# Performance work log

Measured on AMD Instinct MI355X. Metric: run time of the kernel, lower is better.

## Reference

```python
import jax, jax.numpy as jnp
import numpy as np

B, L, D, H = 4, 4096, 2048, 16
HD = D // H  # head_dim = 128
EPS = 1e-9

def phi(x):
    # ELU(x) + 1 : non-negative feature map
    return jax.nn.elu(x) + 1.0

def setup_inputs() -> dict:
    key = jax.random.key(0)
    k1, k2, k3 = jax.random.split(key, 3)
    x = jax.random.normal(k1, (B, L, D), dtype=jnp.float32)
    W_qkv = jax.random.normal(k2, (3 * D, D), dtype=jnp.float32) * (D ** -0.5)
    W_out = jax.random.normal(k3, (D, D), dtype=jnp.float32) * (D ** -0.5)
    return {"x": x, "W_qkv": W_qkv, "W_out": W_out}

def reference(x, W_qkv, W_out):
    b, l, d = x.shape
    qkv = x @ W_qkv.T                      # (B, L, 3D)
    q, k, v = jnp.split(qkv, 3, axis=-1)   # each (B, L, D)
    # (B, L, H, HD) -> (B, H, L, HD)
    q = q.reshape(b, l, H, HD).transpose(0, 2, 1, 3)
    k = k.reshape(b, l, H, HD).transpose(0, 2, 1, 3)
    v = v.reshape(b, l, H, HD).transpose(0, 2, 1, 3)
    q = phi(q)
    k = phi(k)
    kv_cumsum = jnp.cumsum(k * v, axis=2)  # prefix sum over sequence dim
    k_cumsum = jnp.cumsum(k, axis=2)
    out = q * kv_cumsum / (q * k_cumsum + EPS)
    out = out.transpose(0, 2, 1, 3).reshape(b, l, d)
    return (out @ W_out.T) * (HD ** -0.5)
```

## Files before the change

### kernel.cpp

```cpp
#include <hip/hip_runtime.h>
#include <hip/hip_bf16.h>
#include <stdint.h>

#define B_ 4
#define L_ 4096
#define D_ 2048
#define TD_ (3 * D_)
#define CHUNKS 128
#define CLEN (L_ / CHUNKS)
#define M_ (B_ * L_)
#define K_ 2048
#define NT (K_ / 64)

typedef __bf16 bf16x8 __attribute__((ext_vector_type(8)));
typedef float f32x4 __attribute__((ext_vector_type(4)));
typedef ushort u16x8 __attribute__((ext_vector_type(8)));

__device__ __forceinline__ ushort f2bf(float f) {
  uint32_t u = __builtin_bit_cast(uint32_t, f);
  u += 0x7fffu + ((u >> 16) & 1u);
  return (ushort)(u >> 16);
}

__device__ __forceinline__ float bf2f(ushort u) {
  return __builtin_bit_cast(float, (uint32_t)u << 16);
}

__device__ __forceinline__ float phi_f(float x) {
  return x > 0.f ? x + 1.f : __expf(x);
}

__device__ __forceinline__ void gload_lds16(const ushort* g, ushort* l) {
  __builtin_amdgcn_global_load_lds(
      (__attribute__((address_space(1))) void*)(g),
      (__attribute__((address_space(3))) void*)(l), 16, 0, 0);
}

#define SBAR() __builtin_amdgcn_s_barrier()
#define SCHED0() __builtin_amdgcn_sched_barrier(0)
#define MFMA16(a, b, c) __builtin_amdgcn_mfma_f32_16x16x32_bf16((a), (b), (c), 0, 0, 0)

__global__ void cvt_bf16_kernel(const float* __restrict__ in,
                                ushort* __restrict__ out, int n4) {
  int i = blockIdx.x * blockDim.x + threadIdx.x;
  if (i >= n4) return;
  float4 v = reinterpret_cast<const float4*>(in)[i];
  ushort4 o;
  o.x = f2bf(v.x); o.y = f2bf(v.y); o.z = f2bf(v.z); o.w = f2bf(v.w);
  reinterpret_cast<ushort4*>(out)[i] = o;
}

__device__ __forceinline__ void stage_half(const ushort* __restrict__ G,
                                           int row0, int k0, char* lds_half,
                                           int tid) {
#pragma unroll
  for (int lp = 0; lp < 2; ++lp) {
    const int p = lp * 8192 + tid * 16;
    const int row = p >> 7;
    const int cb = (p & 127) ^ ((row & 7) << 4);
    gload_lds16(G + (size_t)(row0 + row) * K_ + k0 + (cb >> 1),
                (ushort*)(lds_half + p));
  }
}

#define RD(p, off) (*reinterpret_cast<const bf16x8*>((p) + (off)))

#define KTILE(t, c)                                                            \
  {                                                                            \
    if ((t) + 1 < NT) {                                                        \
      const int kn = ((t) + 1) * 64;                                           \
      stage_half(A, rA, kn, lsA + (1 - (c)) * 32768, tid);                     \
      stage_half(A, rA + 128, kn, lsA + (1 - (c)) * 32768 + 16384, tid);       \
      stage_half(Bm, rB, kn, lsB + (1 - (c)) * 32768, tid);                    \
      stage_half(Bm, rB + 128, kn, lsB + (1 - (c)) * 32768 + 16384, tid);      \
    }                                                                          \
    SCHED0();                                                                  \
    _Pragma("unroll") for (int i = 0; i < 4; ++i) {                            \
      af[i][0] = RD(bA0, (c) * 32768 + i * 2048);                              \
      af[i][1] = RD(bA1, (c) * 32768 + i * 2048);                              \
    }                                                                          \
    _Pragma("unroll") for (int j = 0; j < 4; ++j) {                            \
      bfr[j][0] = RD(bB0, (c) * 32768 + j * 2048);                             \
      bfr[j][1] = RD(bB1, (c) * 32768 + j * 2048);                             \
    }                                                                          \
    __builtin_amdgcn_s_setprio(1);                                             \
    _Pragma("unroll") for (int ks = 0; ks < 2; ++ks)                           \
    _Pragma("unroll") for (int i = 0; i < 4; ++i)                              \
    _Pragma("unroll") for (int j = 0; j < 4; ++j)                              \
        acc[i][j] = MFMA16(af[i][ks], bfr[j][ks], acc[i][j]);                  \
    __builtin_amdgcn_s_setprio(0);                                             \
    _Pragma("unroll") for (int i = 0; i < 4; ++i) {                            \
      af[i][0] = RD(bA0, (c) * 32768 + 8192 + i * 2048);                       \
      af[i][1] = RD(bA1, (c) * 32768 + 8192 + i * 2048);                       \
    }                                                                          \
    __builtin_amdgcn_s_setprio(1);                                             \
    _Pragma("unroll") for (int ks = 0; ks < 2; ++ks)                           \
    _Pragma("unroll") for (int i = 0; i < 4; ++i)                              \
    _Pragma("unroll") for (int j = 0; j < 4; ++j)                              \
        acc[4 + i][j] = MFMA16(af[i][ks], bfr[j][ks], acc[4 + i][j]);          \
    __builtin_amdgcn_s_setprio(0);                                             \
    SCHED0();                                                                  \
    asm volatile("s_waitcnt vmcnt(0)" ::: "memory");                           \
    SBAR();                                                                    \
    SCHED0();                                                                  \
  }

__device__ __forceinline__ void gemm_core(const ushort* __restrict__ A,
                                          const ushort* __restrict__ Bm,
                                          int bm, int bn, char* ls,
                                          f32x4 (&acc)[8][4]) {
  const int tid = threadIdx.x;
  const int lane = tid & 63, wid = tid >> 6;
  const int wm = (wid >> 2) * 128, wn = (wid & 3) * 64;
  const int l16 = lane & 15, kg = lane >> 4;
  const int rA = bm * 256, rB = bn * 256;

  char* lsA = ls;
  char* lsB = ls + 65536;

  const int v16 = (l16 & 7) << 4;
  const int c0 = (kg * 16) ^ v16;
  const int c1 = (64 + kg * 16) ^ v16;
  const char* bA0 = lsA + (wm + l16) * 128 + c0;
  const char* bA1 = lsA + (wm + l16) * 128 + c1;
  const char* bB0 = lsB + (wn + l16) * 128 + c0;
  const char* bB1 = lsB + (wn + l16) * 128 + c1;

  stage_half(A, rA, 0, lsA, tid);
  stage_half(A, rA + 128, 0, lsA + 16384, tid);
  stage_half(Bm, rB, 0, lsB, tid);
  stage_half(Bm, rB + 128, 0, lsB + 16384, tid);
  asm volatile("s_waitcnt vmcnt(0)" ::: "memory");
  SBAR();
  SCHED0();

  bf16x8 af[4][2], bfr[4][2];
#pragma unroll 1
  for (int t2 = 0; t2 < NT; t2 += 2) {
    KTILE(t2, 0);
    KTILE(t2 + 1, 1);
  }
}

__global__ __launch_bounds__(512, 2) void gemm_qkv8(
    const ushort* __restrict__ A, const ushort* __restrict__ Bm,
    ushort* __restrict__ qb, ushort* __restrict__ kb, ushort* __restrict__ vb) {
  extern __shared__ char ls[];
  const int nwg = gridDim.x;
  const int wg = blockIdx.x;
  const int swz = (wg & 7) * (nwg >> 3) + (wg >> 3);
  const int MT = M_ / 256;
  const int bm = swz % MT, bn = swz / MT;

  f32x4 acc[8][4] = {};
  gemm_core(A, Bm, bm, bn, ls, acc);

  const int seg = bn >> 3;
  ushort* dst = seg == 0 ? qb : (seg == 1 ? kb : vb);
  const int colbase = bn * 256 - seg * 2048;
  const int tid = threadIdx.x;
  const int lane = tid & 63, wid = tid >> 6;
  const int wm = (wid >> 2) * 128, wn = (wid & 3) * 64;
  const int l16 = lane & 15, kg = lane >> 4;
#pragma unroll
  for (int i = 0; i < 8; ++i) {
    const int row0 = bm * 256 + wm + i * 16 + kg * 4;
#pragma unroll
    for (int j = 0; j < 4; ++j) {
      const int col = colbase + wn + j * 16 + l16;
      ushort* cp = dst + (size_t)row0 * D_ + col;
#pragma unroll
      for (int r = 0; r < 4; ++r) cp[(size_t)r * D_] = f2bf(acc[i][j][r]);
    }
  }
}

__global__ __launch_bounds__(512, 2) void gemm_out8(
    const ushort* __restrict__ A, const ushort* __restrict__ Bm,
    float* __restrict__ C, float scale) {
  extern __shared__ char ls[];
  const int nwg = gridDim.x;
  const int wg = blockIdx.x;
  const int swz = (wg & 7) * (nwg >> 3) + (wg >> 3);
  const int MT = M_ / 256;
  const int bm = swz % MT, bn = swz / MT;

  f32x4 acc[8][4] = {};
  gemm_core(A, Bm, bm, bn, ls, acc);

  const int tid = threadIdx.x;
  const int lane = tid & 63, wid = tid >> 6;
  const int wm = (wid >> 2) * 128, wn = (wid & 3) * 64;
  const int l16 = lane & 15, kg = lane >> 4;
#pragma unroll
  for (int i = 0; i < 8; ++i) {
    const int row0 = bm * 256 + wm + i * 16 + kg * 4;
#pragma unroll
    for (int j = 0; j < 4; ++j) {
      const int col = bn * 256 + wn + j * 16 + l16;
      float* cp = C + (size_t)row0 * D_ + col;
#pragma unroll
      for (int r = 0; r < 4; ++r) cp[(size_t)r * D_] = acc[i][j][r] * scale;
    }
  }
}

__global__ void chunk_sums_kernel(const ushort* __restrict__ kb,
                                  const ushort* __restrict__ vb,
                                  float* __restrict__ sums) {
  const int d0 = threadIdx.x * 8;
  const int b = blockIdx.y, c = blockIdx.z;
  float sk[8] = {}, skv[8] = {};
  const size_t rowbase = (size_t)b * L_ + (size_t)c * CLEN;
  for (int l = 0; l < CLEN; ++l) {
    const size_t idx = (rowbase + l) * D_ + d0;
    u16x8 k8 = *reinterpret_cast<const u16x8*>(kb + idx);
    u16x8 v8 = *reinterpret_cast<const u16x8*>(vb + idx);
#pragma unroll
    for (int j = 0; j < 8; ++j) {
      float k = phi_f(bf2f(k8[j]));
      sk[j] += k;
      skv[j] = fmaf(k, bf2f(v8[j]), skv[j]);
    }
  }
  float* s = sums + ((size_t)(b * CHUNKS + c) * 2) * D_ + d0;
#pragma unroll
  for (int j = 0; j < 8; ++j) {
    s[j] = sk[j];
    s[D_ + j] = skv[j];
  }
}

__global__ void chunk_prefix_kernel(float* __restrict__ sums) {
  const int idx = blockIdx.x * 256 + threadIdx.x;
  const int b = idx >> 11, d = idx & (D_ - 1);
  float rk = 0.f, rkv = 0.f;
  for (int c = 0; c < CHUNKS; ++c) {
    float* s = sums + ((size_t)(b * CHUNKS + c) * 2) * D_ + d;
    float sk = s[0], skv = s[D_];
    s[0] = rk;
    s[D_] = rkv;
    rk += sk;
    rkv += skv;
  }
}

__global__ void apply_kernel(const ushort* __restrict__ qb,
                             const ushort* __restrict__ kb,
                             const ushort* __restrict__ vb,
                             const float* __restrict__ sums,
                             ushort* __restrict__ outb) {
  const int d0 = threadIdx.x * 8;
  const int b = blockIdx.y, c = blockIdx.z;
  const float* s = sums + ((size_t)(b * CHUNKS + c) * 2) * D_ + d0;
  float rk[8], rkv[8];
#pragma unroll
  for (int j = 0; j < 8; ++j) {
    rk[j] = s[j];
    rkv[j] = s[D_ + j];
  }
  const size_t rowbase = (size_t)b * L_ + (size_t)c * CLEN;
  for (int l = 0; l < CLEN; ++l) {
    const size_t idx = (rowbase + l) * D_ + d0;
    u16x8 q8 = *reinterpret_cast<const u16x8*>(qb + idx);
    u16x8 k8 = *reinterpret_cast<const u16x8*>(kb + idx);
    u16x8 v8 = *reinterpret_cast<const u16x8*>(vb + idx);
    u16x8 o8;
#pragma unroll
    for (int j = 0; j < 8; ++j) {
      float q = phi_f(bf2f(q8[j]));
      float k = phi_f(bf2f(k8[j]));
      float v = bf2f(v8[j]);
      rkv[j] = fmaf(k, v, rkv[j]);
      rk[j] += k;
      float o = (q * rkv[j]) / fmaf(q, rk[j], 1e-9f);
      o8[j] = f2bf(o);
    }
    *reinterpret_cast<u16x8*>(outb + idx) = o8;
  }
}

extern "C" void kernel_launch(void* const* d_in, const int* in_sizes, int n_in,
                              void* d_out, int out_size, void* d_ws, size_t ws_size,
                              hipStream_t stream) {
  (void)in_sizes; (void)n_in; (void)out_size; (void)ws_size;
  const float* x = (const float*)d_in[0];
  const float* Wqkv = (const float*)d_in[1];
  const float* Wout = (const float*)d_in[2];
  float* out = (float*)d_out;

  ushort* kb = (ushort*)d_out;
  ushort* vb = kb + (size_t)M_ * D_;

  char* ws = (char*)d_ws;
  size_t off = 0;
  auto alloc = [&](size_t bytes) -> void* {
    off = (off + 255) & ~(size_t)255;
    void* p = ws + off;
    off += bytes;
    return p;
  };
  ushort* qb = (ushort*)alloc((size_t)M_ * D_ * 2);
  ushort* xb = (ushort*)alloc((size_t)M_ * D_ * 2);
  ushort* wqb = (ushort*)alloc((size_t)TD_ * D_ * 2);
  ushort* wob = (ushort*)alloc((size_t)D_ * D_ * 2);
  float* sums = (float*)alloc((size_t)B_ * CHUNKS * 2 * D_ * 4);
  ushort* outb = xb;

  (void)hipFuncSetAttribute((const void*)gemm_qkv8,
                            hipFuncAttributeMaxDynamicSharedMemorySize, 131072);
  (void)hipFuncSetAttribute((const void*)gemm_out8,
                            hipFuncAttributeMaxDynamicSharedMemorySize, 131072);

  cvt_bf16_kernel<<<(M_ * D_ / 4 + 255) / 256, 256, 0, stream>>>(x, xb, M_ * D_ / 4);
  cvt_bf16_kernel<<<(TD_ * D_ / 4 + 255) / 256, 256, 0, stream>>>(Wqkv, wqb, TD_ * D_ / 4);
  cvt_bf16_kernel<<<(D_ * D_ / 4 + 255) / 256, 256, 0, stream>>>(Wout, wob, D_ * D_ / 4);

  gemm_qkv8<<<dim3((TD_ / 256) * (M_ / 256)), 512, 131072, stream>>>(xb, wqb, qb, kb, vb);

  chunk_sums_kernel<<<dim3(1, B_, CHUNKS), 256, 0, stream>>>(kb, vb, sums);
  chunk_prefix_kernel<<<dim3(B_ * D_ / 256), 256, 0, stream>>>(sums);
  apply_kernel<<<dim3(1, B_, CHUNKS), 256, 0, stream>>>(qb, kb, vb, sums, outb);

  gemm_out8<<<dim3((D_ / 256) * (M_ / 256)), 512, 131072, stream>>>(outb, wob, out,
                                                                    0.08838834764831845f);
}
```

Baseline: 623.8 us.

## Triple-buffer B tiles in LDS to prefetch two k-steps ahead

The GEMM core now keeps three LDS buffers for the B operand and two for A. B tiles are prefetched two k-steps ahead, and the end-of-iteration wait drops from vmcnt(0) to vmcnt(4), so the newest B loads can stay in flight across the barrier. The intent is to hide more global-load latency behind MFMA work instead of draining every load each iteration. The cost is a dynamic LDS request raised to 160KB, which uses the whole per-CU budget, plus ring-buffer offset bookkeeping and a reordered MFMA loop nest.

```diff
diff --git a/kernel.cpp b/kernel.cpp
--- a/kernel.cpp
+++ b/kernel.cpp
@@ -65,46 +65,6 @@
 
 #define RD(p, off) (*reinterpret_cast<const bf16x8*>((p) + (off)))
 
-#define KTILE(t, c)                                                            \
-  {                                                                            \
-    if ((t) + 1 < NT) {                                                        \
-      const int kn = ((t) + 1) * 64;                                           \
-      stage_half(A, rA, kn, lsA + (1 - (c)) * 32768, tid);                     \
-      stage_half(A, rA + 128, kn, lsA + (1 - (c)) * 32768 + 16384, tid);       \
-      stage_half(Bm, rB, kn, lsB + (1 - (c)) * 32768, tid);                    \
-      stage_half(Bm, rB + 128, kn, lsB + (1 - (c)) * 32768 + 16384, tid);      \
-    }                                                                          \
-    SCHED0();                                                                  \
-    _Pragma("unroll") for (int i = 0; i < 4; ++i) {                            \
-      af[i][0] = RD(bA0, (c) * 32768 + i * 2048);                              \
-      af[i][1] = RD(bA1, (c) * 32768 + i * 2048);                              \
-    }                                                                          \
-    _Pragma("unroll") for (int j = 0; j < 4; ++j) {                            \
-      bfr[j][0] = RD(bB0, (c) * 32768 + j * 2048);                             \
-      bfr[j][1] = RD(bB1, (c) * 32768 + j * 2048);                             \
-    }                                                                          \
-    __builtin_amdgcn_s_setprio(1);                                             \
-    _Pragma("unroll") for (int ks = 0; ks < 2; ++ks)                           \
-    _Pragma("unroll") for (int i = 0; i < 4; ++i)                              \
-    _Pragma("unroll") for (int j = 0; j < 4; ++j)                              \
-        acc[i][j] = MFMA16(af[i][ks], bfr[j][ks], acc[i][j]);                  \
-    __builtin_amdgcn_s_setprio(0);                                             \
-    _Pragma("unroll") for (int i = 0; i < 4; ++i) {                            \
-      af[i][0] = RD(bA0, (c) * 32768 + 8192 + i * 2048);                       \
-      af[i][1] = RD(bA1, (c) * 32768 + 8192 + i * 2048);                       \
-    }                                                                          \
-    __builtin_amdgcn_s_setprio(1);                                             \
-    _Pragma("unroll") for (int ks = 0; ks < 2; ++ks)                           \
-    _Pragma("unroll") for (int i = 0; i < 4; ++i)                              \
-    _Pragma("unroll") for (int j = 0; j < 4; ++j)                              \
-        acc[4 + i][j] = MFMA16(af[i][ks], bfr[j][ks], acc[4 + i][j]);          \
-    __builtin_amdgcn_s_setprio(0);                                             \
-    SCHED0();                                                                  \
-    asm volatile("s_waitcnt vmcnt(0)" ::: "memory");                           \
-    SBAR();                                                                    \
-    SCHED0();                                                                  \
-  }
-
 __device__ __forceinline__ void gemm_core(const ushort* __restrict__ A,
                                           const ushort* __restrict__ Bm,
                                           int bm, int bn, char* ls,
@@ -130,15 +90,81 @@
   stage_half(A, rA + 128, 0, lsA + 16384, tid);
   stage_half(Bm, rB, 0, lsB, tid);
   stage_half(Bm, rB + 128, 0, lsB + 16384, tid);
-  asm volatile("s_waitcnt vmcnt(0)" ::: "memory");
+  stage_half(Bm, rB, 64, lsB + 32768, tid);
+  stage_half(Bm, rB + 128, 64, lsB + 32768 + 16384, tid);
+  asm volatile("s_waitcnt vmcnt(4)" ::: "memory");
   SBAR();
   SCHED0();
 
   bf16x8 af[4][2], bfr[4][2];
+  int caOff = 0;
+  int cbOff = 0;
+
 #pragma unroll 1
-  for (int t2 = 0; t2 < NT; t2 += 2) {
-    KTILE(t2, 0);
-    KTILE(t2 + 1, 1);
+  for (int t = 0; t < NT; ++t) {
+    const int caN = caOff ^ 32768;
+    int cb2 = cbOff + 65536;
+    if (cb2 >= 98304) cb2 -= 98304;
+
+    if (t + 1 < NT) {
+      const int kn = (t + 1) * 64;
+      stage_half(A, rA, kn, lsA + caN, tid);
+      stage_half(A, rA + 128, kn, lsA + caN + 16384, tid);
+    }
+    if (t + 2 < NT) {
+      const int kn2 = (t + 2) * 64;
+      stage_half(Bm, rB, kn2, lsB + cb2, tid);
+      stage_half(Bm, rB + 128, kn2, lsB + cb2 + 16384, tid);
+    }
+    SCHED0();
+
+#pragma unroll
+    for (int i = 0; i < 4; ++i) {
+      af[i][0] = RD(bA0, caOff + i * 2048);
+      af[i][1] = RD(bA1, caOff + i * 2048);
+    }
+#pragma unroll
+    for (int j = 0; j < 4; ++j) {
+      bfr[j][0] = RD(bB0, cbOff + j * 2048);
+      bfr[j][1] = RD(bB1, cbOff + j * 2048);
+    }
+    __builtin_amdgcn_s_setprio(1);
+#pragma unroll
+    for (int i = 0; i < 4; ++i)
+#pragma unroll
+      for (int j = 0; j < 4; ++j)
+#pragma unroll
+        for (int ks = 0; ks < 2; ++ks)
+          acc[i][j] = MFMA16(af[i][ks], bfr[j][ks], acc[i][j]);
+    __builtin_amdgcn_s_setprio(0);
+
+#pragma unroll
+    for (int i = 0; i < 4; ++i) {
+      af[i][0] = RD(bA0, caOff + 8192 + i * 2048);
+      af[i][1] = RD(bA1, caOff + 8192 + i * 2048);
+    }
+    __builtin_amdgcn_s_setprio(1);
+#pragma unroll
+    for (int i = 0; i < 4; ++i)
+#pragma unroll
+      for (int j = 0; j < 4; ++j)
+#pragma unroll
+        for (int ks = 0; ks < 2; ++ks)
+          acc[4 + i][j] = MFMA16(af[i][ks], bfr[j][ks], acc[4 + i][j]);
+    __builtin_amdgcn_s_setprio(0);
+
+    SCHED0();
+    if (t + 2 < NT) {
+      asm volatile("s_waitcnt vmcnt(4)" ::: "memory");
+    } else {
+      asm volatile("s_waitcnt vmcnt(0)" ::: "memory");
+    }
+    SBAR();
+    SCHED0();
+
+    caOff = caN;
+    cbOff += 32768;
+    if (cbOff >= 98304) cbOff -= 98304;
   }
 }
 
@@ -308,20 +334,20 @@
   ushort* outb = xb;
 
   (void)hipFuncSetAttribute((const void*)gemm_qkv8,
-                            hipFuncAttributeMaxDynamicSharedMemorySize, 131072);
+                            hipFuncAttributeMaxDynamicSharedMemorySize, 163840);
   (void)hipFuncSetAttribute((const void*)gemm_out8,
-                            hipFuncAttributeMaxDynamicSharedMemorySize, 131072);
+                            hipFuncAttributeMaxDynamicSharedMemorySize, 163840);
 
   cvt_bf16_kernel<<<(M_ * D_ / 4 + 255) / 256, 256, 0, stream>>>(x, xb, M_ * D_ / 4);
   cvt_bf16_kernel<<<(TD_ * D_ / 4 + 255) / 256, 256, 0, stream>>>(Wqkv, wqb, TD_ * D_ / 4);
   cvt_bf16_kernel<<<(D_ * D_ / 4 + 255) / 256, 256, 0, stream>>>(Wout, wob, D_ * D_ / 4);
 
-  gemm_qkv8<<<dim3((TD_ / 256) * (M_ / 256)), 512, 131072, stream>>>(xb, wqb, qb, kb, vb);
+  gemm_qkv8<<<dim3((TD_ / 256) * (M_ / 256)), 512, 163840, stream>>>(xb, wqb, qb, kb, vb);
 
   chunk_sums_kernel<<<dim3(1, B_, CHUNKS), 256, 0, stream>>>(kb, vb, sums);
   chunk_prefix_kernel<<<dim3(B_ * D_ / 256), 256, 0, stream>>>(sums);
   apply_kernel<<<dim3(1, B_, CHUNKS), 256, 0, stream>>>(qb, kb, vb, sums, outb);
 
-  gemm_out8<<<dim3((D_ / 256) * (M_ / 256)), 512, 131072, stream>>>(outb, wob, out,
+  gemm_out8<<<dim3((D_ / 256) * (M_ / 256)), 512, 163840, stream>>>(outb, wob, out,
                                                                     0.08838834764831845f);
 }
```

Result: no change. 621.3 us (-0.4%).
